# Kernel optimization log

Measured on AMD Instinct MI355X. Metric: run time of the kernel, lower is better.

Reference implementation:

```python
import jax, jax.numpy as jnp
import numpy as np

B, N, F, T, O, K = 4, 4000, 16, 16, 16, 3
LN_EPS = 1e-5


def setup_inputs() -> dict:
    key = jax.random.key(0)
    k = jax.random.split(key, 18)
    rn = lambda i, sh, sc=1.0: jax.random.normal(k[i], sh, dtype=jnp.float32) * np.float32(sc)
    ru = lambda i, sh: jax.random.uniform(k[i], sh, dtype=jnp.float32)
    return {
        "x": rn(0, (B, N, F, T)),
        # scale the random Laplacian so the Chebyshev recurrence stays numerically sane
        "laplacian": rn(1, (N, N), 1.0 / np.sqrt(N)),
        "W1": ru(2, (T,)),
        "W2": rn(3, (F, T)),
        "W3": ru(4, (F,)),
        "bs": ru(5, (1, N, N)),
        "Vs": ru(6, (N, N)),
        "U1": ru(7, (N,)),
        "U2": rn(8, (F, N)),
        "U3": ru(9, (F,)),
        "be": ru(10, (1, T, T)),
        "Ve": ru(11, (T, T)),
        "cheb_w": rn(12, (K, F, O), 1.0 / np.sqrt(F)),
        "time_w": rn(13, (O, F, T), 1.0 / np.sqrt(F * T)),
        "time_b": rn(14, (O,)),
        "ln_g": jnp.ones((N, O), dtype=jnp.float32),
        "ln_b": jnp.zeros((N, O), dtype=jnp.float32),
    }


def reference(x, laplacian, W1, W2, W3, bs, Vs, U1, U2, U3, be, Ve,
              cheb_w, time_w, time_b, ln_g, ln_b):
    # ---- temporal attention: E (B,T,T) ----
    # lhs[b,t] = sum_{n,f} x[b,n,f,t] * U1[n]
    t_lhs = jnp.einsum('bnft,n->bt', x, U1)
    # rhs[b,t] = sum_{n,f,g} x[b,n,f,t] * U2[g,n] * U3[g]
    t_rhs = jnp.einsum('bnft,gn,g->bt', x, U2, U3)
    t_prod = t_lhs[:, :, None] * t_rhs[:, None, :]          # (B,T,T) outer product
    E = jnp.einsum('ts,bsr->btr', Ve, jax.nn.sigmoid(t_prod + be))
    E = jax.nn.softmax(E, axis=-1)

    # apply temporal attention along the time axis: (B,N,F,T)
    x_TAt = jnp.einsum('bts,bnfs->bnft', E, x)

    # ---- spatial attention: S (B,N,N) ----
    s_lhs = jnp.einsum('bnft,t->bnf', x, W1)                 # (B,N,F)
    # faithful to the source ops (valid since F == T here)
    s_rhs = jnp.einsum('bnkt,gk,t->bng', x, W2, W3)          # (B,N,F)
    s_prod = jnp.einsum('bnf,bmf->bnm', s_lhs, s_rhs)        # (B,N,N)
    S = jnp.einsum('nm,bmk->bnk', Vs, jax.nn.sigmoid(s_prod + bs))
    S = jax.nn.softmax(S, axis=-1)

    # spatially attended features for all timesteps at once
    x_SAtt = jnp.einsum('bnm,bmft->bnft', S, x_TAt)          # (B,N,F,T)

    # ---- Chebyshev graph conv over every timestep ----
    Tx0 = x_SAtt
    out = jnp.einsum('bnft,fo->bnot', Tx0, cheb_w[0])
    Tx1 = jnp.einsum('nm,bmft->bnft', laplacian, Tx0)
    out = out + jnp.einsum('bnft,fo->bnot', Tx1, cheb_w[1])
    for kk in range(2, K):
        Tx2 = 2.0 * jnp.einsum('nm,bmft->bnft', laplacian, Tx1) - Tx0
        out = out + jnp.einsum('bnft,fo->bnot', Tx2, cheb_w[kk])
        Tx0, Tx1 = Tx1, Tx2
    spatial_gcn_avg = out.mean(axis=-1)                      # (B,N,O)

    # ---- time conv: Conv2d(in,out,kernel=(1,T)) == full contraction over (F,T) ----
    time_out = jnp.einsum('bnct,oct->bno', x, time_w) + time_b

    # ---- residual (in_channels == out_channels branch) ----
    residual = x[:, :, :, -1]                                # (B,N,O)

    y = spatial_gcn_avg + time_out + residual
    # LayerNorm over the last two dims [N, O]
    mean = y.mean(axis=(1, 2), keepdims=True)
    var = jnp.var(y, axis=(1, 2), keepdims=True)
    y = (y - mean) / jnp.sqrt(var + LN_EPS) * ln_g + ln_b
    return jax.nn.relu(y)
```

## Files before the change

kernel.cpp:

```cpp
#include <hip/hip_runtime.h>
#include <math.h>

#define Bc 4
#define Nn 4000
#define KS 4096
#define NP (16000000 + 4096)

typedef _Float16 half8 __attribute__((ext_vector_type(8)));
typedef float f32x4 __attribute__((ext_vector_type(4)));
typedef unsigned short u16x4 __attribute__((ext_vector_type(4)));

static __device__ __forceinline__ unsigned short f2h(float f) {
  _Float16 h = (_Float16)f;
  unsigned short u;
  __builtin_memcpy(&u, &h, 2);
  return u;
}
static __device__ __forceinline__ float h2f(unsigned short u) {
  _Float16 h;
  __builtin_memcpy(&h, &u, 2);
  return (float)h;
}
static __device__ __forceinline__ void gld16(const void* g, void* l) {
  __builtin_amdgcn_global_load_lds(
      (const __attribute__((address_space(1))) unsigned int*)g,
      (__attribute__((address_space(3))) unsigned int*)l, 16, 0, 0);
}

__global__ __launch_bounds__(256) void k1_trhs(
    const float* __restrict__ x, const float* __restrict__ U1,
    const float* __restrict__ U2, const float* __restrict__ U3,
    float* __restrict__ tl, float* __restrict__ tr) {
  int b = blockIdx.y;
  int tid = threadIdx.x;
  int q = tid & 3;
  int n = blockIdx.x * 64 + (tid >> 2);
  float xs[16];
#pragma unroll
  for (int t = 0; t < 16; ++t) xs[t] = 0.f;
  float c1 = 0.f, c2 = 0.f;
  if (n < Nn) {
    const float* xr = x + ((size_t)b * Nn + n) * 256 + q * 64;
#pragma unroll
    for (int f = 0; f < 4; ++f) {
#pragma unroll
      for (int qq = 0; qq < 4; ++qq) {
        float4 v = *(const float4*)(xr + f * 16 + qq * 4);
        xs[qq * 4 + 0] += v.x; xs[qq * 4 + 1] += v.y;
        xs[qq * 4 + 2] += v.z; xs[qq * 4 + 3] += v.w;
      }
    }
    c1 = U1[n];
#pragma unroll
    for (int g = 0; g < 4; ++g) {
      int gg = q * 4 + g;
      c2 += U2[(size_t)gg * Nn + n] * U3[gg];
    }
  }
#pragma unroll
  for (int m = 1; m < 4; m <<= 1) {
    c2 += __shfl_xor(c2, m, 64);
#pragma unroll
    for (int t = 0; t < 16; ++t) xs[t] += __shfl_xor(xs[t], m, 64);
  }
  float v1[4], v2[4];
#pragma unroll
  for (int i = 0; i < 4; ++i) {
    int t = q * 4 + i;
    v1[i] = c1 * xs[t];
    v2[i] = c2 * xs[t];
  }
#pragma unroll
  for (int off = 4; off < 64; off <<= 1) {
#pragma unroll
    for (int i = 0; i < 4; ++i) {
      v1[i] += __shfl_down(v1[i], off, 64);
      v2[i] += __shfl_down(v2[i], off, 64);
    }
  }
  int lane = tid & 63;
  if (lane < 4) {
#pragma unroll
    for (int i = 0; i < 4; ++i) {
      atomicAdd(&tl[b * 16 + lane * 4 + i], v1[i]);
      atomicAdd(&tr[b * 16 + lane * 4 + i], v2[i]);
    }
  }
}

__global__ __launch_bounds__(256) void k2_eattn(
    const float* __restrict__ tl, const float* __restrict__ tr,
    const float* __restrict__ be, const float* __restrict__ Ve,
    float* __restrict__ ecol) {
  int b = blockIdx.x;
  int tid = threadIdx.x;
  __shared__ float sig[256];
  __shared__ float Em[256];
  int s = tid >> 4, r = tid & 15;
  float z = tl[b * 16 + s] * tr[b * 16 + r] + be[s * 16 + r];
  sig[s * 16 + r] = 1.0f / (1.0f + __expf(-z));
  __syncthreads();
  float e = 0.f;
#pragma unroll
  for (int ss = 0; ss < 16; ++ss) e += Ve[s * 16 + ss] * sig[ss * 16 + r];
  Em[s * 16 + r] = e;
  __syncthreads();
  if (tid < 16) {
    float m = -1e30f;
#pragma unroll
    for (int rr = 0; rr < 16; ++rr) m = fmaxf(m, Em[tid * 16 + rr]);
    float ssum = 0.f;
    float ex[16];
#pragma unroll
    for (int rr = 0; rr < 16; ++rr) { ex[rr] = __expf(Em[tid * 16 + rr] - m); ssum += ex[rr]; }
    float inv = 1.0f / ssum;
#pragma unroll
    for (int rr = 0; rr < 16; ++rr) Em[tid * 16 + rr] = ex[rr] * inv;
  }
  __syncthreads();
  if (tid < 16) {
    float c = 0.f;
#pragma unroll
    for (int tt = 0; tt < 16; ++tt) c += Em[tt * 16 + tid];
    ecol[b * 16 + tid] = c;
  }
}

__global__ __launch_bounds__(256) void k3_pern(
    const float* __restrict__ x, const float* __restrict__ ecol,
    const float* __restrict__ W1, const float* __restrict__ W2,
    const float* __restrict__ W3, const float* __restrict__ time_w,
    const float* __restrict__ time_b,
    float* __restrict__ xts, float* __restrict__ slhs,
    float* __restrict__ srhs, float* __restrict__ base) {
  __shared__ float tws[4096];
  __shared__ float W1s[16], W3s[16], Ecs[16], tbs[16], W2s[256];
  int tid = threadIdx.x;
  int b = blockIdx.y;
  for (int i = tid; i < 4096; i += 256) tws[i] = time_w[i];
  W2s[tid] = W2[tid & 255];
  if (tid < 16) {
    W1s[tid] = W1[tid]; W3s[tid] = W3[tid];
    Ecs[tid] = ecol[b * 16 + tid]; tbs[tid] = time_b[tid];
  }
  __syncthreads();
  int n = blockIdx.x * 256 + tid;
  if (n >= Nn) return;
  const float* xr = x + ((size_t)b * Nn + n) * 256;
  float xtsv[16], slv[16], xw3[16], to[16], resid[16];
#pragma unroll
  for (int i = 0; i < 16; ++i) { xtsv[i] = 0; slv[i] = 0; xw3[i] = 0; to[i] = 0; }
  for (int f = 0; f < 16; ++f) {
    float xf[16];
#pragma unroll
    for (int q = 0; q < 4; ++q) {
      float4 v = *(const float4*)(xr + f * 16 + q * 4);
      xf[q * 4 + 0] = v.x; xf[q * 4 + 1] = v.y; xf[q * 4 + 2] = v.z; xf[q * 4 + 3] = v.w;
    }
    float a = 0, c = 0, d = 0;
#pragma unroll
    for (int t2 = 0; t2 < 16; ++t2) {
      a += Ecs[t2] * xf[t2];
      c += W1s[t2] * xf[t2];
      d += W3s[t2] * xf[t2];
    }
    xtsv[f] = a; slv[f] = c; xw3[f] = d; resid[f] = xf[15];
#pragma unroll
    for (int o = 0; o < 16; ++o) {
      float acc = 0;
#pragma unroll
      for (int t2 = 0; t2 < 16; ++t2) acc += tws[o * 256 + f * 16 + t2] * xf[t2];
      to[o] += acc;
    }
  }
  size_t o16 = ((size_t)b * Nn + n) * 16;
#pragma unroll
  for (int g = 0; g < 16; ++g) {
    float acc = 0;
#pragma unroll
    for (int k2 = 0; k2 < 16; ++k2) acc += W2s[g * 16 + k2] * xw3[k2];
    srhs[o16 + g] = acc;
  }
#pragma unroll
  for (int i = 0; i < 16; ++i) {
    xts[o16 + i] = xtsv[i];
    slhs[o16 + i] = slv[i];
    base[o16 + i] = to[i] + tbs[i] + resid[i];
  }
}

__global__ __launch_bounds__(256) void fconv(
    const float* __restrict__ src, unsigned short* __restrict__ dst) {
  size_t i = ((size_t)blockIdx.x * 256 + threadIdx.x) * 4;
  float4 v = *(const float4*)(src + i);
  u16x4 h;
  h.x = f2h(v.x); h.y = f2h(v.y); h.z = f2h(v.z); h.w = f2h(v.w);
  *(u16x4*)(dst + i) = h;
}

__global__ __launch_bounds__(256) void vconv2(
    const float* __restrict__ Vs, unsigned short* __restrict__ Vh) {
  int row = blockIdx.y;
  int col = blockIdx.x * 1024 + threadIdx.x * 4;
  u16x4 h;
  if (row < Nn && col < Nn) {
    float4 v = *(const float4*)(Vs + (size_t)row * Nn + col);
    h.x = f2h(v.x); h.y = f2h(v.y); h.z = f2h(v.z); h.w = f2h(v.w);
  } else {
    h.x = 0; h.y = 0; h.z = 0; h.w = 0;
  }
  *(u16x4*)(Vh + (size_t)row * KS + col) = h;
}

__global__ __launch_bounds__(256) void tsconv(
    const float* __restrict__ ts, unsigned short* __restrict__ tsT) {
  int n = blockIdx.x * 256 + threadIdx.x;
  int col = blockIdx.y;
  if (n >= Nn) return;
  int b = col >> 4, f = col & 15;
  tsT[(size_t)col * Nn + n] = f2h(ts[((size_t)b * Nn + n) * 16 + f]);
}

__global__ __launch_bounds__(256) void gemm1_P(
    const float* __restrict__ slhs, const float* __restrict__ srhs,
    const unsigned short* __restrict__ bsH, unsigned short* __restrict__ PhT, int b) {
  __shared__ float Ms[64][17];
  __shared__ float Cs[64][17];
  __shared__ float Pt[64][65];
  int tid = threadIdx.x;
  int m0 = blockIdx.y * 64, k0 = blockIdx.x * 64;
  int lr = tid >> 2, lq = (tid & 3) << 2;
  {
    int gm = m0 + lr; if (gm > Nn - 1) gm = Nn - 1;
    float4 v = *(const float4*)(slhs + ((size_t)b * Nn + gm) * 16 + lq);
    Ms[lr][lq + 0] = v.x; Ms[lr][lq + 1] = v.y; Ms[lr][lq + 2] = v.z; Ms[lr][lq + 3] = v.w;
    int gk = k0 + lr; if (gk > Nn - 1) gk = Nn - 1;
    float4 w = *(const float4*)(srhs + ((size_t)b * Nn + gk) * 16 + lq);
    Cs[lr][lq + 0] = w.x; Cs[lr][lq + 1] = w.y; Cs[lr][lq + 2] = w.z; Cs[lr][lq + 3] = w.w;
  }
  __syncthreads();
  int tx = tid & 15, ty = tid >> 4;
  float acc[4][4] = {};
#pragma unroll
  for (int f = 0; f < 16; ++f) {
    float a4[4], b4[4];
#pragma unroll
    for (int i = 0; i < 4; ++i) a4[i] = Ms[ty * 4 + i][f];
#pragma unroll
    for (int j = 0; j < 4; ++j) b4[j] = Cs[tx * 4 + j][f];
#pragma unroll
    for (int i = 0; i < 4; ++i)
#pragma unroll
      for (int j = 0; j < 4; ++j) acc[i][j] += a4[i] * b4[j];
  }
#pragma unroll
  for (int i = 0; i < 4; ++i) {
    int m = m0 + ty * 4 + i;
    int k = k0 + tx * 4;
    float bv[4] = {0.f, 0.f, 0.f, 0.f};
    if (m < Nn) {
      if (k + 3 < Nn) {
        u16x4 t4 = *(const u16x4*)(bsH + (size_t)m * Nn + k);
        bv[0] = h2f(t4.x); bv[1] = h2f(t4.y); bv[2] = h2f(t4.z); bv[3] = h2f(t4.w);
      } else {
        for (int j = 0; j < 4; ++j)
          if (k + j < Nn) bv[j] = h2f(bsH[(size_t)m * Nn + k + j]);
      }
    }
#pragma unroll
    for (int j = 0; j < 4; ++j) {
      float z = acc[i][j] + bv[j];
      Pt[ty * 4 + i][tx * 4 + j] = 1.f / (1.f + __expf(-z));
    }
  }
  __syncthreads();
#pragma unroll
  for (int i = 0; i < 4; ++i) {
    int kl = ty * 4 + i;
    int ml = tx * 4;
    int gm = m0 + ml;
    u16x4 h;
    h.x = f2h(Pt[ml + 0][kl]);
    h.y = f2h(Pt[ml + 1][kl]);
    h.z = f2h(Pt[ml + 2][kl]);
    h.w = f2h(Pt[ml + 3][kl]);
    size_t off = (size_t)(k0 + kl) * KS + gm;
    if (gm + 3 < Nn) {
      *(u16x4*)(PhT + off) = h;
    } else {
      unsigned short hv[4] = {h.x, h.y, h.z, h.w};
      for (int q = 0; q < 4; ++q)
        if (gm + q < Nn) PhT[off + q] = hv[q];
    }
  }
}

__global__ __launch_bounds__(512, 2) void gemm2_mfma(
    const unsigned short* __restrict__ Vh, const unsigned short* __restrict__ PhT,
    float* __restrict__ SP, unsigned int* __restrict__ rmaxu) {
  __shared__ unsigned short Ah[2][2][8192];
  __shared__ unsigned short Bh[2][2][8192];
  int t = threadIdx.x;
  int bid = blockIdx.x;
  int wg = (bid & 7) * 32 + (bid >> 3);
  int row0 = (wg >> 4) * 256, col0 = (wg & 15) * 256;

  int sr = t >> 2, sg = t & 3;
  int ssw = sg ^ ((t >> 3) & 3);
  size_t a0 = (size_t)(row0 + sr) * KS + ssw * 8;
  size_t a1 = (size_t)(row0 + 128 + sr) * KS + ssw * 8;
  size_t b0 = (size_t)(col0 + sr) * KS + ssw * 8;
  size_t b1 = (size_t)(col0 + 128 + sr) * KS + ssw * 8;
  int ld0 = t * 8, ld1 = 4096 + t * 8;

  int lane = t & 63, wid = t >> 6;
  int wm = (wid >> 2) * 128, wn = (wid & 3) * 64;
  int ml = lane & 15, qd = lane >> 4;
  int gr = qd ^ ((ml >> 1) & 3);
  int aro[8], bro[4];
#pragma unroll
  for (int i = 0; i < 8; ++i) aro[i] = (wm + ml + i * 16) * 32 + gr * 8;
#pragma unroll
  for (int j = 0; j < 4; ++j) bro[j] = (wn + ml + j * 16) * 32 + gr * 8;

  f32x4 acc[8][4] = {};

#define STG(P, X, bf, kh, o0, o1, kt)                          \
  do {                                                         \
    size_t c_ = (size_t)(kt) * 64 + (kh) * 32;                 \
    gld16(P + (o0) + c_, &X[bf][kh][ld0]);                     \
    gld16(P + (o1) + c_, &X[bf][kh][ld1]);                     \
  } while (0)

  STG(Vh, Ah, 0, 0, a0, a1, 0); STG(PhT, Bh, 0, 0, b0, b1, 0);
  STG(Vh, Ah, 0, 1, a0, a1, 0); STG(PhT, Bh, 0, 1, b0, b1, 0);
  STG(Vh, Ah, 1, 0, a0, a1, 1); STG(PhT, Bh, 1, 0, b0, b1, 1);
  STG(Vh, Ah, 1, 1, a0, a1, 1); STG(PhT, Bh, 1, 1, b0, b1, 1);
  asm volatile("s_waitcnt vmcnt(12)" ::: "memory");
  __builtin_amdgcn_s_barrier();

#define PH_MFMA_BEGIN()                                        \
  __builtin_amdgcn_s_barrier();                                \
  asm volatile("s_waitcnt lgkmcnt(0)" ::: "memory");           \
  __builtin_amdgcn_sched_barrier(0);                           \
  __builtin_amdgcn_s_setprio(1)

#pragma unroll 1
  for (int G = 0; G < 64; ++G) {
    int cb = G & 1, nb = cb ^ 1;
    int tn1 = (G + 1 < 64) ? G + 1 : 63;
    int tn2 = (G + 2 < 64) ? G + 2 : 63;
    half8 av[4], bv[4];
#pragma unroll
    for (int j = 0; j < 4; ++j) bv[j] = *(const half8*)&Bh[cb][0][bro[j]];
#pragma unroll
    for (int i = 0; i < 4; ++i) av[i] = *(const half8*)&Ah[cb][0][aro[i]];
    STG(Vh, Ah, nb, 1, a0, a1, tn1);
    PH_MFMA_BEGIN();
#pragma unroll
    for (int i = 0; i < 4; ++i)
#pragma unroll
      for (int j = 0; j < 4; ++j)
        acc[i][j] = __builtin_amdgcn_mfma_f32_16x16x32_f16(av[i], bv[j], acc[i][j], 0, 0, 0);
    __builtin_amdgcn_s_setprio(0);
    __builtin_amdgcn_s_barrier();
#pragma unroll
    for (int i = 0; i < 4; ++i) av[i] = *(const half8*)&Ah[cb][0][aro[4 + i]];
    STG(PhT, Bh, nb, 1, b0, b1, tn1);
    PH_MFMA_BEGIN();
#pragma unroll
    for (int i = 0; i < 4; ++i)
#pragma unroll
      for (int j = 0; j < 4; ++j)
        acc[4 + i][j] = __builtin_amdgcn_mfma_f32_16x16x32_f16(av[i], bv[j], acc[4 + i][j], 0, 0, 0);
    __builtin_amdgcn_s_setprio(0);
    asm volatile("s_waitcnt vmcnt(8)" ::: "memory");
    __builtin_amdgcn_s_barrier();
#pragma unroll
    for (int j = 0; j < 4; ++j) bv[j] = *(const half8*)&Bh[cb][1][bro[j]];
#pragma unroll
    for (int i = 0; i < 4; ++i) av[i] = *(const half8*)&Ah[cb][1][aro[i]];
    STG(Vh, Ah, cb, 0, a0, a1, tn2);
    PH_MFMA_BEGIN();
#pragma unroll
    for (int i = 0; i < 4; ++i)
#pragma unroll
      for (int j = 0; j < 4; ++j)
        acc[i][j] = __builtin_amdgcn_mfma_f32_16x16x32_f16(av[i], bv[j], acc[i][j], 0, 0, 0);
    __builtin_amdgcn_s_setprio(0);
    __builtin_amdgcn_s_barrier();
#pragma unroll
    for (int i = 0; i < 4; ++i) av[i] = *(const half8*)&Ah[cb][1][aro[4 + i]];
    STG(PhT, Bh, cb, 0, b0, b1, tn2);
    PH_MFMA_BEGIN();
#pragma unroll
    for (int i = 0; i < 4; ++i)
#pragma unroll
      for (int j = 0; j < 4; ++j)
        acc[4 + i][j] = __builtin_amdgcn_mfma_f32_16x16x32_f16(av[i], bv[j], acc[4 + i][j], 0, 0, 0);
    __builtin_amdgcn_s_setprio(0);
    asm volatile("s_waitcnt vmcnt(8)" ::: "memory");
    __builtin_amdgcn_s_barrier();
  }
#undef STG
#undef PH_MFMA_BEGIN

#pragma unroll
  for (int i = 0; i < 8; ++i) {
#pragma unroll
    for (int r = 0; r < 4; ++r) {
      int grow = row0 + wm + i * 16 + qd * 4 + r;
      if (grow >= Nn) continue;
      float rowmax = -3.0e38f;
#pragma unroll
      for (int j = 0; j < 4; ++j) {
        int gcol = col0 + wn + j * 16 + ml;
        if (gcol < Nn) {
          float v = acc[i][j][r];
          SP[(size_t)grow * Nn + gcol] = v;
          rowmax = fmaxf(rowmax, v);
        }
      }
#pragma unroll
      for (int mk = 1; mk < 16; mk <<= 1)
        rowmax = fmaxf(rowmax, __shfl_xor(rowmax, mk, 64));
      if (ml == 0) {
        unsigned u = __float_as_uint(rowmax);
        u = (u & 0x80000000u) ? ~u : (u | 0x80000000u);
        atomicMax(rmaxu + grow, u);
      }
    }
  }
}

__global__ __launch_bounds__(256) void txsum_sp(
    const float* __restrict__ SP, const float* __restrict__ xts,
    const unsigned int* __restrict__ rmaxu, float* __restrict__ lsum,
    float* __restrict__ ts0, int b) {
  __shared__ float Ws[16][65];
  __shared__ float Xs[64][17];
  int tid = threadIdx.x;
  int n0 = blockIdx.x * 16;
  int kbase = blockIdx.y * 1000, kend = kbase + 1000;
  int r = tid >> 4, f = tid & 15;
  int lq = f * 4;
  int xr = tid >> 2, xc = (tid & 3) << 2;
  const float* spr = SP + (size_t)(n0 + r) * Nn;
  unsigned u = rmaxu[n0 + r];
  u = (u & 0x80000000u) ? (u ^ 0x80000000u) : ~u;
  float rm = __uint_as_float(u);
  float acc = 0.f, lpart = 0.f;
  for (int k0 = kbase; k0 < kend; k0 += 64) {
    int gx = k0 + xr;
    if (gx < kend) {
      float4 v = *(const float4*)(xts + ((size_t)b * Nn + gx) * 16 + xc);
      Xs[xr][xc + 0] = v.x; Xs[xr][xc + 1] = v.y; Xs[xr][xc + 2] = v.z; Xs[xr][xc + 3] = v.w;
    } else {
      Xs[xr][xc + 0] = 0.f; Xs[xr][xc + 1] = 0.f; Xs[xr][xc + 2] = 0.f; Xs[xr][xc + 3] = 0.f;
    }
    int gk = k0 + lq;
    float4 v = *(const float4*)(spr + gk);
    float e0 = (gk + 0 < kend) ? __expf(v.x - rm) : 0.f;
    float e1 = (gk + 1 < kend) ? __expf(v.y - rm) : 0.f;
    float e2 = (gk + 2 < kend) ? __expf(v.z - rm) : 0.f;
    float e3 = (gk + 3 < kend) ? __expf(v.w - rm) : 0.f;
    Ws[r][lq + 0] = e0; Ws[r][lq + 1] = e1; Ws[r][lq + 2] = e2; Ws[r][lq + 3] = e3;
    lpart += e0 + e1 + e2 + e3;
    __syncthreads();
#pragma unroll
    for (int kk = 0; kk < 64; ++kk) acc += Ws[r][kk] * Xs[kk][f];
    __syncthreads();
  }
#pragma unroll
  for (int mk = 1; mk < 16; mk <<= 1) lpart += __shfl_xor(lpart, mk, 64);
  if (f == 0) atomicAdd(&lsum[n0 + r], lpart);
  atomicAdd(&ts0[((size_t)b * Nn + n0 + r) * 16 + f], acc);
}

__global__ __launch_bounds__(256) void nrm_k(
    float* __restrict__ ts0, const float* __restrict__ lsum) {
  int tid = threadIdx.x;
  int b = blockIdx.y;
  int n = blockIdx.x * 16 + (tid >> 4);
  size_t i = ((size_t)b * Nn + n) * 16 + (tid & 15);
  ts0[i] = ts0[i] / lsum[b * Nn + n];
}

__global__ __launch_bounds__(256) void chebm(
    const unsigned short* __restrict__ lapH, const unsigned short* __restrict__ tsT,
    float* __restrict__ Cout) {
  __shared__ unsigned short Ah[64 * 32];
  __shared__ unsigned short Bh[64 * 32];
  int t = threadIdx.x;
  int row0 = blockIdx.x * 64;
  int kc0 = blockIdx.y * 25 * 32;
  int kc1 = kc0 + 25 * 32;
  int arow = row0 + (t >> 2); if (arow > Nn - 1) arow = Nn - 1;
  size_t a_base = (size_t)arow * Nn + (t & 3) * 8;
  size_t b_base = (size_t)(t >> 2) * Nn + (t & 3) * 8;

  int lane = t & 63;
  int wid = t >> 6;
  int wm = (wid >> 1) * 32, wn = (wid & 1) * 32;
  int ml = lane & 15, qd = lane >> 4;
  int aoff = (wm + ml) * 32 + qd * 8;
  int boff = (wn + ml) * 32 + qd * 8;

  f32x4 acc[2][2] = {};

  for (int k0 = kc0; k0 < kc1; k0 += 32) {
    gld16(lapH + a_base + k0, &Ah[t * 8]);
    gld16(tsT + b_base + k0, &Bh[t * 8]);
    __syncthreads();
    half8 a_h[2], b_h[2];
#pragma unroll
    for (int i = 0; i < 2; ++i) a_h[i] = *(const half8*)&Ah[aoff + i * 512];
#pragma unroll
    for (int j = 0; j < 2; ++j) b_h[j] = *(const half8*)&Bh[boff + j * 512];
#pragma unroll
    for (int i = 0; i < 2; ++i)
#pragma unroll
      for (int j = 0; j < 2; ++j)
        acc[i][j] = __builtin_amdgcn_mfma_f32_16x16x32_f16(a_h[i], b_h[j], acc[i][j], 0, 0, 0);
    __syncthreads();
  }
#pragma unroll
  for (int i = 0; i < 2; ++i)
#pragma unroll
    for (int j = 0; j < 2; ++j) {
      int gcol = wn + j * 16 + ml;
      int b = gcol >> 4, f = gcol & 15;
#pragma unroll
      for (int r = 0; r < 4; ++r) {
        int grow = row0 + wm + i * 16 + qd * 4 + r;
        if (grow < Nn) {
          size_t idx = ((size_t)b * Nn + grow) * 16 + f;
          atomicAdd(&Cout[idx], acc[i][j][r]);
        }
      }
    }
}

__global__ __launch_bounds__(256) void ky_k(
    const float* __restrict__ ts0, const float* __restrict__ ts1,
    const float* __restrict__ ts2, const float* __restrict__ cw,
    const float* __restrict__ base, float* __restrict__ ybuf,
    float* __restrict__ lnacc) {
  __shared__ float T0[256], T1[256], T2[256], CW[768];
  __shared__ float rs[256], rq[256];
  int tid = threadIdx.x;
  int b = blockIdx.y;
  size_t base_i = ((size_t)b * Nn + blockIdx.x * 16) * 16;
  T0[tid] = ts0[base_i + tid];
  T1[tid] = ts1[base_i + tid];
  T2[tid] = ts2[base_i + tid];
  for (int i = tid; i < 768; i += 256) CW[i] = cw[i];
  __syncthreads();
  int r = tid >> 4, o = tid & 15;
  float acc = 0.f;
#pragma unroll
  for (int f2 = 0; f2 < 16; ++f2) {
    float c2 = CW[512 + f2 * 16 + o];
    acc += T0[r * 16 + f2] * (CW[f2 * 16 + o] - c2);
    acc += T1[r * 16 + f2] * CW[256 + f2 * 16 + o];
    acc += (2.0f * T2[r * 16 + f2]) * c2;
  }
  float y = acc * 0.0625f + base[base_i + tid];
  ybuf[base_i + tid] = y;
  rs[tid] = y; rq[tid] = y * y;
  __syncthreads();
  for (int s2 = 128; s2 > 0; s2 >>= 1) {
    if (tid < s2) { rs[tid] += rs[tid + s2]; rq[tid] += rq[tid + s2]; }
    __syncthreads();
  }
  if (tid == 0) {
    atomicAdd(&lnacc[b * 2 + 0], rs[0]);
    atomicAdd(&lnacc[b * 2 + 1], rq[0]);
  }
}

__global__ __launch_bounds__(256) void kln_k(
    const float* __restrict__ ybuf, const float* __restrict__ lnacc,
    const float* __restrict__ lg, const float* __restrict__ lb,
    float* __restrict__ outp) {
  int tid = threadIdx.x;
  int b = blockIdx.y;
  size_t i = ((size_t)b * Nn + blockIdx.x * 16) * 16 + tid;
  size_t nz = (size_t)blockIdx.x * 256 + tid;
  const float inv = 1.0f / 64000.0f;
  float s = lnacc[b * 2 + 0], q = lnacc[b * 2 + 1];
  float mean = s * inv;
  float var = q * inv - mean * mean;
  float rstd = rsqrtf(var + 1e-5f);
  float v = (ybuf[i] - mean) * rstd * lg[nz] + lb[nz];
  outp[i] = fmaxf(v, 0.f);
}

extern "C" void kernel_launch(void* const* d_in, const int* in_sizes, int n_in,
                              void* d_out, int out_size, void* d_ws, size_t ws_size,
                              hipStream_t stream) {
  const float* x   = (const float*)d_in[0];
  const float* lap = (const float*)d_in[1];
  const float* W1  = (const float*)d_in[2];
  const float* W2  = (const float*)d_in[3];
  const float* W3  = (const float*)d_in[4];
  const float* bs  = (const float*)d_in[5];
  const float* Vs  = (const float*)d_in[6];
  const float* U1  = (const float*)d_in[7];
  const float* U2  = (const float*)d_in[8];
  const float* U3  = (const float*)d_in[9];
  const float* be  = (const float*)d_in[10];
  const float* Ve  = (const float*)d_in[11];
  const float* cw  = (const float*)d_in[12];
  const float* tw  = (const float*)d_in[13];
  const float* tb  = (const float*)d_in[14];
  const float* lg  = (const float*)d_in[15];
  const float* lb  = (const float*)d_in[16];
  float* ws = (float*)d_ws;
  float* SP = ws;
  unsigned short* Vh   = (unsigned short*)(ws + (size_t)NP);
  unsigned short* PhT  = Vh + (size_t)KS * KS;
  unsigned short* lapH = PhT + (size_t)KS * KS;
  unsigned short* bsH  = lapH + (size_t)Nn * Nn;
  unsigned short* tsT  = bsH + (size_t)Nn * Nn;
  float* xts  = (float*)(tsT + 64 * Nn + 64);
  float* slhs = xts + 256000;
  float* srhs = slhs + 256000;
  float* base = srhs + 256000;
  float* ts0  = base + 256000;
  float* ts1  = ts0 + 256000;
  float* ts2  = ts1 + 256000;
  float* ybuf = ts2 + 256000;
  float* tl   = ybuf + 256000;
  float* tr   = tl + 64;
  float* ecol = tr + 64;
  unsigned int* rmaxu = (unsigned int*)(ecol + 64);
  float* lsum = (float*)(rmaxu + Bc * Nn);
  float* lnacc = lsum + Bc * Nn;

  hipMemsetAsync(tl, 0, 128 * sizeof(float), stream);
  hipMemsetAsync(lnacc, 0, 8 * sizeof(float), stream);
  hipMemsetAsync(ts0, 0, 256000 * sizeof(float), stream);
  hipMemsetAsync(ts1, 0, 256000 * sizeof(float), stream);
  hipMemsetAsync(ts2, 0, 256000 * sizeof(float), stream);
  hipMemsetAsync(rmaxu, 0, Bc * Nn * sizeof(unsigned int), stream);
  hipMemsetAsync(lsum, 0, Bc * Nn * sizeof(float), stream);

  k1_trhs<<<dim3(63, 4), 256, 0, stream>>>(x, U1, U2, U3, tl, tr);
  k2_eattn<<<dim3(4), 256, 0, stream>>>(tl, tr, be, Ve, ecol);
  k3_pern<<<dim3(16, 4), 256, 0, stream>>>(x, ecol, W1, W2, W3, tw, tb,
                                           xts, slhs, srhs, base);
  vconv2<<<dim3(4, 4096), 256, 0, stream>>>(Vs, Vh);
  fconv<<<dim3(15625), 256, 0, stream>>>(lap, lapH);
  fconv<<<dim3(15625), 256, 0, stream>>>(bs, bsH);
  for (int b = 0; b < 4; ++b) {
    gemm1_P<<<dim3(63, 63), 256, 0, stream>>>(slhs, srhs, bsH, PhT, b);
    gemm2_mfma<<<dim3(256), 512, 0, stream>>>(Vh, PhT, SP, rmaxu + b * Nn);
    txsum_sp<<<dim3(250, 4), 256, 0, stream>>>(SP, xts, rmaxu + b * Nn,
                                               lsum + b * Nn, ts0, b);
  }
  nrm_k<<<dim3(250, 4), 256, 0, stream>>>(ts0, lsum);
  tsconv<<<dim3(16, 64), 256, 0, stream>>>(ts0, tsT);
  chebm<<<dim3(63, 5), 256, 0, stream>>>(lapH, tsT, ts1);
  tsconv<<<dim3(16, 64), 256, 0, stream>>>(ts1, tsT);
  chebm<<<dim3(63, 5), 256, 0, stream>>>(lapH, tsT, ts2);
  ky_k<<<dim3(250, 4), 256, 0, stream>>>(ts0, ts1, ts2, cw, base, ybuf, lnacc);
  kln_k<<<dim3(250, 4), 256, 0, stream>>>(ybuf, lnacc, lg, lb, (float*)d_out);
}
```

Baseline: 1.225 ms.

## Use fp16 MFMA for softmax-weighted spatial aggregation in txsum_sp

Rewrites txsum_sp so each wave computes exp(SP - rowmax) for 16 rows and multiplies it against an fp16 transposed copy of xts held in LDS, using 16x16x32 f16 MFMA instructions instead of scalar FMAs over shared-memory tiles. The grid changes to 64 rows by 800-column chunks, so the whole xts chunk is staged once per block and the per-iteration barriers go away. The goal is to cut the FMA and LDS cost of this N x N x 16 reduction. In exchange, the exp weights and x values are rounded to half precision, which adds error, and the edge rows now need clamping and bounds checks.

New measurement: 1.136 ms. -7.3%, faster.

```diff
diff --git a/kernel.cpp b/kernel.cpp
--- a/kernel.cpp
+++ b/kernel.cpp
@@ -437,44 +437,52 @@
     const float* __restrict__ SP, const float* __restrict__ xts,
     const unsigned int* __restrict__ rmaxu, float* __restrict__ lsum,
     float* __restrict__ ts0, int b) {
-  __shared__ float Ws[16][65];
-  __shared__ float Xs[64][17];
-  int tid = threadIdx.x;
-  int n0 = blockIdx.x * 16;
-  int kbase = blockIdx.y * 1000, kend = kbase + 1000;
-  int r = tid >> 4, f = tid & 15;
-  int lq = f * 4;
-  int xr = tid >> 2, xc = (tid & 3) << 2;
-  const float* spr = SP + (size_t)(n0 + r) * Nn;
-  unsigned u = rmaxu[n0 + r];
+  __shared__ unsigned short XT[16][824];
+  int tid = threadIdx.x;
+  int kbase = blockIdx.y * 800;
+  for (int i4 = tid; i4 < 3200; i4 += 256) {
+    int k = i4 >> 2, f4 = (i4 & 3) << 2;
+    float4 v = *(const float4*)(xts + ((size_t)b * Nn + kbase + k) * 16 + f4);
+    XT[f4 + 0][k] = f2h(v.x); XT[f4 + 1][k] = f2h(v.y);
+    XT[f4 + 2][k] = f2h(v.z); XT[f4 + 3][k] = f2h(v.w);
+  }
+  __syncthreads();
+  int lane = tid & 63, wid = tid >> 6;
+  int ml = lane & 15, qd = lane >> 4;
+  int n0 = blockIdx.x * 64 + wid * 16;
+  int nr = n0 + ml;
+  int nrc = nr < Nn ? nr : Nn - 1;
+  unsigned u = rmaxu[nrc];
   u = (u & 0x80000000u) ? (u ^ 0x80000000u) : ~u;
   float rm = __uint_as_float(u);
-  float acc = 0.f, lpart = 0.f;
-  for (int k0 = kbase; k0 < kend; k0 += 64) {
-    int gx = k0 + xr;
-    if (gx < kend) {
-      float4 v = *(const float4*)(xts + ((size_t)b * Nn + gx) * 16 + xc);
-      Xs[xr][xc + 0] = v.x; Xs[xr][xc + 1] = v.y; Xs[xr][xc + 2] = v.z; Xs[xr][xc + 3] = v.w;
-    } else {
-      Xs[xr][xc + 0] = 0.f; Xs[xr][xc + 1] = 0.f; Xs[xr][xc + 2] = 0.f; Xs[xr][xc + 3] = 0.f;
-    }
-    int gk = k0 + lq;
-    float4 v = *(const float4*)(spr + gk);
-    float e0 = (gk + 0 < kend) ? __expf(v.x - rm) : 0.f;
-    float e1 = (gk + 1 < kend) ? __expf(v.y - rm) : 0.f;
-    float e2 = (gk + 2 < kend) ? __expf(v.z - rm) : 0.f;
-    float e3 = (gk + 3 < kend) ? __expf(v.w - rm) : 0.f;
-    Ws[r][lq + 0] = e0; Ws[r][lq + 1] = e1; Ws[r][lq + 2] = e2; Ws[r][lq + 3] = e3;
-    lpart += e0 + e1 + e2 + e3;
-    __syncthreads();
-#pragma unroll
-    for (int kk = 0; kk < 64; ++kk) acc += Ws[r][kk] * Xs[kk][f];
-    __syncthreads();
-  }
-#pragma unroll
-  for (int mk = 1; mk < 16; mk <<= 1) lpart += __shfl_xor(lpart, mk, 64);
-  if (f == 0) atomicAdd(&lsum[n0 + r], lpart);
-  atomicAdd(&ts0[((size_t)b * Nn + n0 + r) * 16 + f], acc);
+  const float* spr = SP + (size_t)nrc * Nn + kbase + qd * 8;
+  f32x4 acc = {0.f, 0.f, 0.f, 0.f};
+  float lpart = 0.f;
+#pragma unroll 1
+  for (int ks = 0; ks < 25; ++ks) {
+    float4 v0 = *(const float4*)(spr + ks * 32);
+    float4 v1 = *(const float4*)(spr + ks * 32 + 4);
+    float e0 = __expf(v0.x - rm), e1 = __expf(v0.y - rm);
+    float e2 = __expf(v0.z - rm), e3 = __expf(v0.w - rm);
+    float e4 = __expf(v1.x - rm), e5 = __expf(v1.y - rm);
+    float e6 = __expf(v1.z - rm), e7 = __expf(v1.w - rm);
+    lpart += ((e0 + e1) + (e2 + e3)) + ((e4 + e5) + (e6 + e7));
+    half8 a_h, b_h;
+    a_h[0] = (_Float16)e0; a_h[1] = (_Float16)e1;
+    a_h[2] = (_Float16)e2; a_h[3] = (_Float16)e3;
+    a_h[4] = (_Float16)e4; a_h[5] = (_Float16)e5;
+    a_h[6] = (_Float16)e6; a_h[7] = (_Float16)e7;
+    b_h = *(const half8*)&XT[ml][ks * 32 + qd * 8];
+    acc = __builtin_amdgcn_mfma_f32_16x16x32_f16(a_h, b_h, acc, 0, 0, 0);
+  }
+  lpart += __shfl_xor(lpart, 16, 64);
+  lpart += __shfl_xor(lpart, 32, 64);
+  if (qd == 0 && nr < Nn) atomicAdd(&lsum[nr], lpart);
+#pragma unroll
+  for (int r = 0; r < 4; ++r) {
+    int n = n0 + qd * 4 + r;
+    if (n < Nn) atomicAdd(&ts0[((size_t)b * Nn + n) * 16 + ml], acc[r]);
+  }
 }
 
 __global__ __launch_bounds__(256) void nrm_k(
@@ -656,8 +664,8 @@
   for (int b = 0; b < 4; ++b) {
     gemm1_P<<<dim3(63, 63), 256, 0, stream>>>(slhs, srhs, bsH, PhT, b);
     gemm2_mfma<<<dim3(256), 512, 0, stream>>>(Vh, PhT, SP, rmaxu + b * Nn);
-    txsum_sp<<<dim3(250, 4), 256, 0, stream>>>(SP, xts, rmaxu + b * Nn,
-                                               lsum + b * Nn, ts0, b);
+    txsum_sp<<<dim3(63, 5), 256, 0, stream>>>(SP, xts, rmaxu + b * Nn,
+                                              lsum + b * Nn, ts0, b);
   }
   nrm_k<<<dim3(250, 4), 256, 0, stream>>>(ts0, lsum);
   tsconv<<<dim3(16, 64), 256, 0, stream>>>(ts0, tsT);
```
